# Optimization experiments

Measured on AMD Instinct MI355X. Metric: run time of the kernel, lower is better.

The kernel has to match this reference:

```python
import jax, jax.numpy as jnp
import numpy as np

ALPHA = 0.2  # leaky relu slope
NEG = -9e15

N, NFEAT, NHID, NHEADS = 4096, 1024, 64, 8
EMB = NHID * NHEADS  # 512


def setup_inputs() -> dict:
    key = jax.random.key(0)
    ks = jax.random.split(key, 16)
    x = jax.random.normal(ks[0], (N, NFEAT), dtype=jnp.float32)
    adj = (jax.random.uniform(ks[1], (N, N)) < 0.01).astype(jnp.float32)
    adj = jnp.maximum(adj, jnp.eye(N, dtype=jnp.float32))
    s = 0.05
    W = jax.random.normal(ks[2], (NHEADS, NFEAT, NHID), dtype=jnp.float32) * s
    a1 = jax.random.normal(ks[3], (NHEADS, NHID), dtype=jnp.float32) * s
    a2 = jax.random.normal(ks[4], (NHEADS, NHID), dtype=jnp.float32) * s
    # decoder: 512 -> 256 -> 256 -> 512 -> 1024 (PyTorch Linear convention: y = x @ W.T + b)
    W1 = jax.random.normal(ks[5], (EMB // 2, EMB), dtype=jnp.float32) * s
    b1 = jnp.zeros((EMB // 2,), dtype=jnp.float32)
    W2 = jax.random.normal(ks[6], (NFEAT // 4, EMB // 2), dtype=jnp.float32) * s
    b2 = jnp.zeros((NFEAT // 4,), dtype=jnp.float32)
    W3 = jax.random.normal(ks[7], (NFEAT // 2, NFEAT // 4), dtype=jnp.float32) * s
    b3 = jnp.zeros((NFEAT // 2,), dtype=jnp.float32)
    W4 = jax.random.normal(ks[8], (NFEAT, NFEAT // 2), dtype=jnp.float32) * s
    b4 = jnp.zeros((NFEAT,), dtype=jnp.float32)
    return {"x": x, "adj": adj, "W": W, "a1": a1, "a2": a2,
            "W1": W1, "b1": b1, "W2": W2, "b2": b2,
            "W3": W3, "b3": b3, "W4": W4, "b4": b4}


def reference(x, adj, W, a1, a2, W1, b1, W2, b2, W3, b3, W4, b4):
    # --- encoder: multi-head GAT (dropout=0) ---
    Wh = jnp.einsum('nf,hfd->hnd', x, W)              # [H, N, nhid]
    e_src = jnp.einsum('hnd,hd->hn', Wh, a1)          # [H, N]
    e_dst = jnp.einsum('hnd,hd->hn', Wh, a2)          # [H, N]
    e = jax.nn.leaky_relu(e_src[:, :, None] + e_dst[:, None, :], ALPHA)  # [H, N, N]
    e = jnp.where(adj[None] > 0, e, NEG)
    att = jax.nn.softmax(e, axis=-1)
    h = jnp.einsum('hnm,hmd->hnd', att, Wh)           # [H, N, nhid]
    h = jax.nn.elu(h)                                 # concat=True -> elu per layer
    enc = jnp.transpose(h, (1, 0, 2)).reshape(x.shape[0], -1)  # [N, H*nhid]
    # --- decoder: 4-layer MLP ---
    out = jax.nn.relu(enc @ W1.T + b1)
    out = jax.nn.relu(out @ W2.T + b2)
    out = jax.nn.relu(out @ W3.T + b3)
    out = out @ W4.T + b4
    return out
```

## Files before the change

kernel.cpp:

```cpp
#include <hip/hip_runtime.h>
#include <hip/hip_bf16.h>
#include <math.h>

#define NNODES 4096
#define NFEAT_ 1024
#define NHID_  64
#define NHEADS_ 8
#define EMB_   512
#define MAXD   256
constexpr float ALPHA_ = 0.2f;

typedef __attribute__((ext_vector_type(8))) short bf16x8;
typedef __attribute__((ext_vector_type(4))) float f32x4;
typedef unsigned int u32;
typedef unsigned short u16;

__device__ inline u16 f2b(float f) {
    __hip_bfloat16 b = __float2bfloat16(f);
    return *(u16*)&b;
}
__device__ inline float b2f(u16 u) {
    return __uint_as_float(((u32)u) << 16);
}

__device__ inline void cp16(const void* g, void* l) {
    __builtin_amdgcn_global_load_lds(
        (const __attribute__((address_space(1))) u32*)g,
        (__attribute__((address_space(3))) u32*)l, 16, 0, 0);
}

template<int BM, int BN, int OUTM, int ACT, bool SCORES>
__global__ __launch_bounds__(256) void gemm_bt(
    const u16* __restrict__ A, const u16* __restrict__ B,
    const float* __restrict__ bias, void* __restrict__ Cv,
    const float* __restrict__ a1, const float* __restrict__ a2,
    float* __restrict__ es, float* __restrict__ edT,
    int M, int N, int K)
{
    constexpr int BK  = 32;
    constexpr int WM  = BM / 2;
    constexpr int MI  = WM / 16;
    constexpr int WN  = BN / 2;
    constexpr int NJ  = WN / 16;
    constexpr int ACH = BM / 16;
    constexpr int BCH = BN / 16;
    static_assert(!SCORES || BN == 64, "SCORES assumes one head per block");

    __shared__ __align__(16) u16 As[2][BM * BK];
    __shared__ __align__(16) u16 Bs[2][BN * BK];
    __shared__ float s1Lds[SCORES ? 2 : 1][SCORES ? BM : 1];
    __shared__ float s2Lds[SCORES ? 2 : 1][SCORES ? BM : 1];

    const int tid  = threadIdx.x;
    const int wid  = tid >> 6, lane = tid & 63;
    const int wr   = wid >> 1, wc = wid & 1;
    const int m0   = blockIdx.y * BM, n0 = blockIdx.x * BN;
    const int frow = lane & 15, fk = (lane >> 4) * 8;
    const int lr   = lane >> 2, lc = (lane & 3) * 8;

    auto stage = [&](int buf, int k0) {
        const u16* gA = A + (long)m0 * K + k0;
        {
            int c = wid;
            cp16(gA + (long)(c * 16 + lr) * K + lc, &As[buf][c * 512]);
            if (ACH == 8) {
                c = wid + 4;
                cp16(gA + (long)(c * 16 + lr) * K + lc, &As[buf][c * 512]);
            }
        }
        const u16* gB = B + (long)n0 * K + k0;
        if (BCH >= 4) {
            int c = wid;
            cp16(gB + (long)(c * 16 + lr) * K + lc, &Bs[buf][c * 512]);
            if (BCH == 8) {
                c = wid + 4;
                cp16(gB + (long)(c * 16 + lr) * K + lc, &Bs[buf][c * 512]);
            }
        } else if (wid < BCH) {
            cp16(gB + (long)(wid * 16 + lr) * K + lc, &Bs[buf][wid * 512]);
        }
    };

    f32x4 acc[MI][NJ] = {};

    stage(0, 0);
    __syncthreads();
    int cur = 0;
    for (int k0 = 0; k0 < K; k0 += BK) {
        if (k0 + BK < K) stage(cur ^ 1, k0 + BK);

        bf16x8 af[MI], bfr[NJ];
        #pragma unroll
        for (int i = 0; i < MI; ++i)
            af[i] = *(const bf16x8*)&As[cur][(wr * WM + i * 16 + frow) * BK + fk];
        #pragma unroll
        for (int j = 0; j < NJ; ++j)
            bfr[j] = *(const bf16x8*)&Bs[cur][(wc * WN + j * 16 + frow) * BK + fk];
        #pragma unroll
        for (int i = 0; i < MI; ++i)
            #pragma unroll
            for (int j = 0; j < NJ; ++j)
                acc[i][j] = __builtin_amdgcn_mfma_f32_16x16x32_bf16(
                    af[i], bfr[j], acc[i][j], 0, 0, 0);

        __syncthreads();
        cur ^= 1;
    }

    const int crow0 = m0 + wr * WM + (lane >> 4) * 4;
    const int ccol0 = n0 + wc * WN + (lane & 15);
    #pragma unroll
    for (int i = 0; i < MI; ++i)
        #pragma unroll
        for (int j = 0; j < NJ; ++j)
            #pragma unroll
            for (int r = 0; r < 4; ++r) {
                const int row = crow0 + i * 16 + r;
                const int col = ccol0 + j * 16;
                float v = acc[i][j][r];
                if (bias) v += bias[col];
                if (ACT == 1) v = v > 0.f ? v : 0.f;
                if (OUTM == 1) ((u16*)Cv)[(long)row * N + col] = f2b(v);
                else           ((float*)Cv)[(long)row * N + col] = v;
            }

    if constexpr (SCORES) {
        const int h = n0 >> 6;
        const float a1v0 = a1[h * 64 + wc * WN + frow];
        const float a1v1 = a1[h * 64 + wc * WN + 16 + frow];
        const float a2v0 = a2[h * 64 + wc * WN + frow];
        const float a2v1 = a2[h * 64 + wc * WN + 16 + frow];
        #pragma unroll
        for (int i = 0; i < MI; ++i)
            #pragma unroll
            for (int r = 0; r < 4; ++r) {
                float s1 = acc[i][0][r] * a1v0 + acc[i][1][r] * a1v1;
                float s2 = acc[i][0][r] * a2v0 + acc[i][1][r] * a2v1;
                #pragma unroll
                for (int off = 8; off; off >>= 1) {
                    s1 += __shfl_xor(s1, off);
                    s2 += __shfl_xor(s2, off);
                }
                if (frow == 0) {
                    const int row = wr * WM + i * 16 + (lane >> 4) * 4 + r;
                    s1Lds[wc][row] = s1;
                    s2Lds[wc][row] = s2;
                }
            }
        __syncthreads();
        if (tid < BM) {
            es[h * NNODES + m0 + tid] = s1Lds[0][tid] + s1Lds[1][tid];
            edT[(m0 + tid) * NHEADS_ + h] = s2Lds[0][tid] + s2Lds[1][tid];
        }
    }
}

#define CASTB 512
__global__ __launch_bounds__(256) void prep_nbr(
    const float* __restrict__ x,   const float* __restrict__ adj,
    const float* __restrict__ W,
    const float* __restrict__ W1,  const float* __restrict__ W2,
    const float* __restrict__ W3,  const float* __restrict__ W4,
    u16* __restrict__ xb,  u16* __restrict__ WcT,
    u16* __restrict__ W1b, u16* __restrict__ W2b,
    u16* __restrict__ W3b, u16* __restrict__ W4b,
    int* __restrict__ cnt, int* __restrict__ nbr)
{
    const int b = blockIdx.x, tid = threadIdx.x;

    if (b < CASTB) {
        const int np = CASTB * 256;
        const int t = b * 256 + tid;
        for (int i = t; i < (NNODES * NFEAT_) / 4; i += np) {
            const float4 v = ((const float4*)x)[i];
            ushort4 o; o.x = f2b(v.x); o.y = f2b(v.y); o.z = f2b(v.z); o.w = f2b(v.w);
            ((ushort4*)xb)[i] = o;
        }
        for (int i = t; i < (256 * 512) / 4; i += np) {
            const float4 v = ((const float4*)W1)[i];
            ushort4 o; o.x = f2b(v.x); o.y = f2b(v.y); o.z = f2b(v.z); o.w = f2b(v.w);
            ((ushort4*)W1b)[i] = o;
        }
        for (int i = t; i < (256 * 256) / 4; i += np) {
            const float4 v = ((const float4*)W2)[i];
            ushort4 o; o.x = f2b(v.x); o.y = f2b(v.y); o.z = f2b(v.z); o.w = f2b(v.w);
            ((ushort4*)W2b)[i] = o;
        }
        for (int i = t; i < (512 * 256) / 4; i += np) {
            const float4 v = ((const float4*)W3)[i];
            ushort4 o; o.x = f2b(v.x); o.y = f2b(v.y); o.z = f2b(v.z); o.w = f2b(v.w);
            ((ushort4*)W3b)[i] = o;
        }
        for (int i = t; i < (1024 * 512) / 4; i += np) {
            const float4 v = ((const float4*)W4)[i];
            ushort4 o; o.x = f2b(v.x); o.y = f2b(v.y); o.z = f2b(v.z); o.w = f2b(v.w);
            ((ushort4*)W4b)[i] = o;
        }
    } else if (b < CASTB + 128) {
        __shared__ float tile[64][65];
        const int tb = b - CASTB;
        const int h = tb >> 4, k0 = (tb & 15) * 64;
        #pragma unroll
        for (int p = 0; p < 4; ++p) {
            const int kr = p * 16 + (tid >> 4), d = (tid & 15) * 4;
            const float4 v = *(const float4*)&W[((long)h * NFEAT_ + k0 + kr) * NHID_ + d];
            tile[kr][d] = v.x; tile[kr][d + 1] = v.y;
            tile[kr][d + 2] = v.z; tile[kr][d + 3] = v.w;
        }
        __syncthreads();
        #pragma unroll
        for (int p = 0; p < 4; ++p) {
            const int d = p * 16 + (tid >> 4), k = (tid & 15) * 4;
            ushort4 o;
            o.x = f2b(tile[k][d]);     o.y = f2b(tile[k + 1][d]);
            o.z = f2b(tile[k + 2][d]); o.w = f2b(tile[k + 3][d]);
            *(ushort4*)&WcT[((long)h * 64 + d) * NFEAT_ + k0 + k] = o;
        }
    } else {
        __shared__ int lcnt;
        const int n = b - CASTB - 128;
        if (tid == 0) lcnt = 0;
        __syncthreads();
        const float4* arow = (const float4*)(adj + (long)n * NNODES);
        for (int m4 = tid; m4 < NNODES / 4; m4 += 256) {
            const float4 v = arow[m4];
            if (v.x != 0.f) { const int p = atomicAdd(&lcnt, 1); if (p < MAXD) nbr[n * MAXD + p] = m4 * 4; }
            if (v.y != 0.f) { const int p = atomicAdd(&lcnt, 1); if (p < MAXD) nbr[n * MAXD + p] = m4 * 4 + 1; }
            if (v.z != 0.f) { const int p = atomicAdd(&lcnt, 1); if (p < MAXD) nbr[n * MAXD + p] = m4 * 4 + 2; }
            if (v.w != 0.f) { const int p = atomicAdd(&lcnt, 1); if (p < MAXD) nbr[n * MAXD + p] = m4 * 4 + 3; }
        }
        __syncthreads();
        if (tid == 0) cnt[n] = lcnt < MAXD ? lcnt : MAXD;
    }
}

__global__ __launch_bounds__(512) void attn_agg(
    const u16* __restrict__ Whb, const float* __restrict__ esrc,
    const float* __restrict__ edT, const int* __restrict__ cnt,
    const int* __restrict__ nbr, u16* __restrict__ enc)
{
    __shared__ __align__(16) int   mLds[MAXD];
    __shared__ __align__(16) float pLds[NHEADS_][MAXD];
    const int h = threadIdx.x >> 6, lane = threadIdx.x & 63;
    const int n = blockIdx.x;

    const int deg  = min(cnt[n], MAXD);
    const int degp = (deg + 15) & ~15;

    if (h == 0) {
        const int* lst = nbr + n * MAXD;
        for (int j = lane; j < deg; j += 64) mLds[j] = lst[j];
        for (int j = deg + lane; j < degp; j += 64) mLds[j] = 0;
    }
    __syncthreads();

    const float es = esrc[h * NNODES + n];

    float mymax = -3.4e38f;
    for (int j = lane; j < deg; j += 64) {
        float ev = es + edT[mLds[j] * NHEADS_ + h];
        ev = ev > 0.f ? ev : ALPHA_ * ev;
        pLds[h][j] = ev;
        mymax = fmaxf(mymax, ev);
    }
    for (int j = deg + lane; j < degp; j += 64) pLds[h][j] = 0.f;
    #pragma unroll
    for (int off = 32; off; off >>= 1) mymax = fmaxf(mymax, __shfl_xor(mymax, off));

    float mysum = 0.f;
    for (int j = lane; j < deg; j += 64) {
        const float p = __expf(pLds[h][j] - mymax);
        pLds[h][j] = p;
        mysum += p;
    }
    #pragma unroll
    for (int off = 32; off; off >>= 1) mysum += __shfl_xor(mysum, off);

    __syncthreads();

    float acc = 0.f;
    const u16* base = Whb + h * NHID_ + lane;
    for (int j0 = 0; j0 < degp; j0 += 16) {
        const int4   ma = *(const int4*)&mLds[j0];
        const int4   mb = *(const int4*)&mLds[j0 + 4];
        const int4   mc = *(const int4*)&mLds[j0 + 8];
        const int4   md = *(const int4*)&mLds[j0 + 12];
        const float4 pa = *(const float4*)&pLds[h][j0];
        const float4 pb = *(const float4*)&pLds[h][j0 + 4];
        const float4 pc = *(const float4*)&pLds[h][j0 + 8];
        const float4 pd = *(const float4*)&pLds[h][j0 + 12];
        const float v0  = b2f(base[(long)ma.x << 9]);
        const float v1  = b2f(base[(long)ma.y << 9]);
        const float v2  = b2f(base[(long)ma.z << 9]);
        const float v3  = b2f(base[(long)ma.w << 9]);
        const float v4  = b2f(base[(long)mb.x << 9]);
        const float v5  = b2f(base[(long)mb.y << 9]);
        const float v6  = b2f(base[(long)mb.z << 9]);
        const float v7  = b2f(base[(long)mb.w << 9]);
        const float v8  = b2f(base[(long)mc.x << 9]);
        const float v9  = b2f(base[(long)mc.y << 9]);
        const float v10 = b2f(base[(long)mc.z << 9]);
        const float v11 = b2f(base[(long)mc.w << 9]);
        const float v12 = b2f(base[(long)md.x << 9]);
        const float v13 = b2f(base[(long)md.y << 9]);
        const float v14 = b2f(base[(long)md.z << 9]);
        const float v15 = b2f(base[(long)md.w << 9]);
        acc = fmaf(pa.x, v0,  acc); acc = fmaf(pa.y, v1,  acc);
        acc = fmaf(pa.z, v2,  acc); acc = fmaf(pa.w, v3,  acc);
        acc = fmaf(pb.x, v4,  acc); acc = fmaf(pb.y, v5,  acc);
        acc = fmaf(pb.z, v6,  acc); acc = fmaf(pb.w, v7,  acc);
        acc = fmaf(pc.x, v8,  acc); acc = fmaf(pc.y, v9,  acc);
        acc = fmaf(pc.z, v10, acc); acc = fmaf(pc.w, v11, acc);
        acc = fmaf(pd.x, v12, acc); acc = fmaf(pd.y, v13, acc);
        acc = fmaf(pd.z, v14, acc); acc = fmaf(pd.w, v15, acc);
    }

    float hv = acc / mysum;
    hv = hv > 0.f ? hv : expm1f(hv);
    enc[(long)n * EMB_ + h * NHID_ + lane] = f2b(hv);
}

extern "C" void kernel_launch(void* const* d_in, const int* in_sizes, int n_in,
                              void* d_out, int out_size, void* d_ws, size_t ws_size,
                              hipStream_t stream)
{
    const float* x   = (const float*)d_in[0];
    const float* adj = (const float*)d_in[1];
    const float* W   = (const float*)d_in[2];
    const float* a1  = (const float*)d_in[3];
    const float* a2  = (const float*)d_in[4];
    const float* W1  = (const float*)d_in[5];
    const float* b1  = (const float*)d_in[6];
    const float* W2  = (const float*)d_in[7];
    const float* b2  = (const float*)d_in[8];
    const float* W3  = (const float*)d_in[9];
    const float* b3  = (const float*)d_in[10];
    const float* W4  = (const float*)d_in[11];
    const float* b4  = (const float*)d_in[12];
    float* out = (float*)d_out;

    float* es  = (float*)d_ws;
    float* edT = es + 32768;
    u16* Whb = (u16*)(edT + 32768);
    u16* enc = Whb + 2097152;
    u16* WcT = enc + 2097152;
    u16* W1b = WcT + 524288;
    u16* W2b = W1b + 131072;
    u16* W3b = W2b + 65536;
    u16* W4b = W3b + 131072;
    int* cnt = (int*)(W4b + 524288);
    int* nbr = cnt + 4096;
    u16* xb  = (u16*)(nbr + 1048576);
    u16* dd1 = xb;
    u16* dd2 = dd1 + 1048576;
    u16* dd3 = dd2 + 1048576;

    prep_nbr<<<dim3(CASTB + 128 + NNODES), 256, 0, stream>>>(
        x, adj, W, W1, W2, W3, W4, xb, WcT, W1b, W2b, W3b, W4b, cnt, nbr);

    gemm_bt<64, 64, 1, 0, true><<<dim3(8, 64), 256, 0, stream>>>(
        xb, WcT, nullptr, Whb, a1, a2, es, edT, NNODES, EMB_, NFEAT_);

    attn_agg<<<dim3(NNODES), 512, 0, stream>>>(Whb, es, edT, cnt, nbr, enc);

    gemm_bt<64, 32, 1, 1, false><<<dim3(8, 64), 256, 0, stream>>>(
        enc, W1b, b1, dd1, nullptr, nullptr, nullptr, nullptr, NNODES, 256, 512);
    gemm_bt<64, 32, 1, 1, false><<<dim3(8, 64), 256, 0, stream>>>(
        dd1, W2b, b2, dd2, nullptr, nullptr, nullptr, nullptr, NNODES, 256, 256);
    gemm_bt<64, 64, 1, 1, false><<<dim3(8, 64), 256, 0, stream>>>(
        dd2, W3b, b3, dd3, nullptr, nullptr, nullptr, nullptr, NNODES, 512, 256);
    gemm_bt<128, 128, 0, 0, false><<<dim3(8, 32), 256, 0, stream>>>(
        dd3, W4b, b4, out, nullptr, nullptr, nullptr, nullptr, NNODES, 1024, 512);
}
```

Baseline: 228.3 us.

## Move adjacency neighbor scan into head GEMM kernel and retile final decoder GEMM

```diff
diff --git a/kernel.cpp b/kernel.cpp
--- a/kernel.cpp
+++ b/kernel.cpp
@@ -29,12 +29,10 @@
         (__attribute__((address_space(3))) u32*)l, 16, 0, 0);
 }
 
-template<int BM, int BN, int OUTM, int ACT, bool SCORES>
+template<int BM, int BN, int OUTM, int ACT>
 __global__ __launch_bounds__(256) void gemm_bt(
     const u16* __restrict__ A, const u16* __restrict__ B,
     const float* __restrict__ bias, void* __restrict__ Cv,
-    const float* __restrict__ a1, const float* __restrict__ a2,
-    float* __restrict__ es, float* __restrict__ edT,
     int M, int N, int K)
 {
     constexpr int BK  = 32;
@@ -44,12 +42,9 @@
     constexpr int NJ  = WN / 16;
     constexpr int ACH = BM / 16;
     constexpr int BCH = BN / 16;
-    static_assert(!SCORES || BN == 64, "SCORES assumes one head per block");
 
     __shared__ __align__(16) u16 As[2][BM * BK];
     __shared__ __align__(16) u16 Bs[2][BN * BK];
-    __shared__ float s1Lds[SCORES ? 2 : 1][SCORES ? BM : 1];
-    __shared__ float s2Lds[SCORES ? 2 : 1][SCORES ? BM : 1];
 
     const int tid  = threadIdx.x;
     const int wid  = tid >> 6, lane = tid & 63;
@@ -123,102 +118,31 @@
                 if (OUTM == 1) ((u16*)Cv)[(long)row * N + col] = f2b(v);
                 else           ((float*)Cv)[(long)row * N + col] = v;
             }
-
-    if constexpr (SCORES) {
-        const int h = n0 >> 6;
-        const float a1v0 = a1[h * 64 + wc * WN + frow];
-        const float a1v1 = a1[h * 64 + wc * WN + 16 + frow];
-        const float a2v0 = a2[h * 64 + wc * WN + frow];
-        const float a2v1 = a2[h * 64 + wc * WN + 16 + frow];
-        #pragma unroll
-        for (int i = 0; i < MI; ++i)
-            #pragma unroll
-            for (int r = 0; r < 4; ++r) {
-                float s1 = acc[i][0][r] * a1v0 + acc[i][1][r] * a1v1;
-                float s2 = acc[i][0][r] * a2v0 + acc[i][1][r] * a2v1;
-                #pragma unroll
-                for (int off = 8; off; off >>= 1) {
-                    s1 += __shfl_xor(s1, off);
-                    s2 += __shfl_xor(s2, off);
-                }
-                if (frow == 0) {
-                    const int row = wr * WM + i * 16 + (lane >> 4) * 4 + r;
-                    s1Lds[wc][row] = s1;
-                    s2Lds[wc][row] = s2;
-                }
-            }
-        __syncthreads();
-        if (tid < BM) {
-            es[h * NNODES + m0 + tid] = s1Lds[0][tid] + s1Lds[1][tid];
-            edT[(m0 + tid) * NHEADS_ + h] = s2Lds[0][tid] + s2Lds[1][tid];
-        }
-    }
-}
-
-#define CASTB 512
-__global__ __launch_bounds__(256) void prep_nbr(
-    const float* __restrict__ x,   const float* __restrict__ adj,
-    const float* __restrict__ W,
-    const float* __restrict__ W1,  const float* __restrict__ W2,
-    const float* __restrict__ W3,  const float* __restrict__ W4,
-    u16* __restrict__ xb,  u16* __restrict__ WcT,
-    u16* __restrict__ W1b, u16* __restrict__ W2b,
-    u16* __restrict__ W3b, u16* __restrict__ W4b,
-    int* __restrict__ cnt, int* __restrict__ nbr)
+}
+
+__global__ __launch_bounds__(256) void head_gemm_nbr(
+    const u16* __restrict__ A, const u16* __restrict__ B,
+    u16* __restrict__ Whb,
+    const float* __restrict__ a1, const float* __restrict__ a2,
+    float* __restrict__ es, float* __restrict__ edT,
+    const float* __restrict__ adj, int* __restrict__ cnt,
+    int* __restrict__ nbr)
 {
-    const int b = blockIdx.x, tid = threadIdx.x;
-
-    if (b < CASTB) {
-        const int np = CASTB * 256;
-        const int t = b * 256 + tid;
-        for (int i = t; i < (NNODES * NFEAT_) / 4; i += np) {
-            const float4 v = ((const float4*)x)[i];
-            ushort4 o; o.x = f2b(v.x); o.y = f2b(v.y); o.z = f2b(v.z); o.w = f2b(v.w);
-            ((ushort4*)xb)[i] = o;
-        }
-        for (int i = t; i < (256 * 512) / 4; i += np) {
-            const float4 v = ((const float4*)W1)[i];
-            ushort4 o; o.x = f2b(v.x); o.y = f2b(v.y); o.z = f2b(v.z); o.w = f2b(v.w);
-            ((ushort4*)W1b)[i] = o;
-        }
-        for (int i = t; i < (256 * 256) / 4; i += np) {
-            const float4 v = ((const float4*)W2)[i];
-            ushort4 o; o.x = f2b(v.x); o.y = f2b(v.y); o.z = f2b(v.z); o.w = f2b(v.w);
-            ((ushort4*)W2b)[i] = o;
-        }
-        for (int i = t; i < (512 * 256) / 4; i += np) {
-            const float4 v = ((const float4*)W3)[i];
-            ushort4 o; o.x = f2b(v.x); o.y = f2b(v.y); o.z = f2b(v.z); o.w = f2b(v.w);
-            ((ushort4*)W3b)[i] = o;
-        }
-        for (int i = t; i < (1024 * 512) / 4; i += np) {
-            const float4 v = ((const float4*)W4)[i];
-            ushort4 o; o.x = f2b(v.x); o.y = f2b(v.y); o.z = f2b(v.z); o.w = f2b(v.w);
-            ((ushort4*)W4b)[i] = o;
-        }
-    } else if (b < CASTB + 128) {
-        __shared__ float tile[64][65];
-        const int tb = b - CASTB;
-        const int h = tb >> 4, k0 = (tb & 15) * 64;
-        #pragma unroll
-        for (int p = 0; p < 4; ++p) {
-            const int kr = p * 16 + (tid >> 4), d = (tid & 15) * 4;
-            const float4 v = *(const float4*)&W[((long)h * NFEAT_ + k0 + kr) * NHID_ + d];
-            tile[kr][d] = v.x; tile[kr][d + 1] = v.y;
-            tile[kr][d + 2] = v.z; tile[kr][d + 3] = v.w;
-        }
-        __syncthreads();
-        #pragma unroll
-        for (int p = 0; p < 4; ++p) {
-            const int d = p * 16 + (tid >> 4), k = (tid & 15) * 4;
-            ushort4 o;
-            o.x = f2b(tile[k][d]);     o.y = f2b(tile[k + 1][d]);
-            o.z = f2b(tile[k + 2][d]); o.w = f2b(tile[k + 3][d]);
-            *(ushort4*)&WcT[((long)h * 64 + d) * NFEAT_ + k0 + k] = o;
-        }
-    } else {
-        __shared__ int lcnt;
-        const int n = b - CASTB - 128;
+    constexpr int BM = 64, BN = 64, BK = 32;
+    constexpr int WM = 32, MI = 2, WN = 32, NJ = 2;
+    constexpr int M = NNODES, N = EMB_, K = NFEAT_;
+
+    __shared__ __align__(16) u16 As[2][BM * BK];
+    __shared__ __align__(16) u16 Bs[2][BN * BK];
+    __shared__ float s1Lds[2][BM];
+    __shared__ float s2Lds[2][BM];
+    __shared__ int lcnt;
+
+    const int bid = blockIdx.x;
+    const int tid = threadIdx.x;
+
+    if (bid >= 512) {
+        const int n = bid - 512;
         if (tid == 0) lcnt = 0;
         __syncthreads();
         const float4* arow = (const float4*)(adj + (long)n * NNODES);
@@ -231,6 +155,147 @@
         }
         __syncthreads();
         if (tid == 0) cnt[n] = lcnt < MAXD ? lcnt : MAXD;
+        return;
+    }
+
+    const int wid  = tid >> 6, lane = tid & 63;
+    const int wr   = wid >> 1, wc = wid & 1;
+    const int m0   = (bid >> 3) * BM, n0 = (bid & 7) * BN;
+    const int frow = lane & 15, fk = (lane >> 4) * 8;
+    const int lr   = lane >> 2, lc = (lane & 3) * 8;
+
+    auto stage = [&](int buf, int k0) {
+        const u16* gA = A + (long)m0 * K + k0;
+        cp16(gA + (long)(wid * 16 + lr) * K + lc, &As[buf][wid * 512]);
+        const u16* gB = B + (long)n0 * K + k0;
+        cp16(gB + (long)(wid * 16 + lr) * K + lc, &Bs[buf][wid * 512]);
+    };
+
+    f32x4 acc[MI][NJ] = {};
+
+    stage(0, 0);
+    __syncthreads();
+    int cur = 0;
+    for (int k0 = 0; k0 < K; k0 += BK) {
+        if (k0 + BK < K) stage(cur ^ 1, k0 + BK);
+
+        bf16x8 af[MI], bfr[NJ];
+        #pragma unroll
+        for (int i = 0; i < MI; ++i)
+            af[i] = *(const bf16x8*)&As[cur][(wr * WM + i * 16 + frow) * BK + fk];
+        #pragma unroll
+        for (int j = 0; j < NJ; ++j)
+            bfr[j] = *(const bf16x8*)&Bs[cur][(wc * WN + j * 16 + frow) * BK + fk];
+        #pragma unroll
+        for (int i = 0; i < MI; ++i)
+            #pragma unroll
+            for (int j = 0; j < NJ; ++j)
+                acc[i][j] = __builtin_amdgcn_mfma_f32_16x16x32_bf16(
+                    af[i], bfr[j], acc[i][j], 0, 0, 0);
+
+        __syncthreads();
+        cur ^= 1;
+    }
+
+    const int crow0 = m0 + wr * WM + (lane >> 4) * 4;
+    const int ccol0 = n0 + wc * WN + (lane & 15);
+    #pragma unroll
+    for (int i = 0; i < MI; ++i)
+        #pragma unroll
+        for (int j = 0; j < NJ; ++j)
+            #pragma unroll
+            for (int r = 0; r < 4; ++r)
+                Whb[(long)(crow0 + i * 16 + r) * N + ccol0 + j * 16] =
+                    f2b(acc[i][j][r]);
+
+    const int h = n0 >> 6;
+    const float a1v0 = a1[h * 64 + wc * WN + frow];
+    const float a1v1 = a1[h * 64 + wc * WN + 16 + frow];
+    const float a2v0 = a2[h * 64 + wc * WN + frow];
+    const float a2v1 = a2[h * 64 + wc * WN + 16 + frow];
+    #pragma unroll
+    for (int i = 0; i < MI; ++i)
+        #pragma unroll
+        for (int r = 0; r < 4; ++r) {
+            float s1 = acc[i][0][r] * a1v0 + acc[i][1][r] * a1v1;
+            float s2 = acc[i][0][r] * a2v0 + acc[i][1][r] * a2v1;
+            #pragma unroll
+            for (int off = 8; off; off >>= 1) {
+                s1 += __shfl_xor(s1, off);
+                s2 += __shfl_xor(s2, off);
+            }
+            if (frow == 0) {
+                const int row = wr * WM + i * 16 + (lane >> 4) * 4 + r;
+                s1Lds[wc][row] = s1;
+                s2Lds[wc][row] = s2;
+            }
+        }
+    __syncthreads();
+    if (tid < BM) {
+        es[h * NNODES + m0 + tid] = s1Lds[0][tid] + s1Lds[1][tid];
+        edT[(m0 + tid) * NHEADS_ + h] = s2Lds[0][tid] + s2Lds[1][tid];
+    }
+}
+
+#define CASTB 512
+__global__ __launch_bounds__(256) void prep(
+    const float* __restrict__ x,   const float* __restrict__ W,
+    const float* __restrict__ W1,  const float* __restrict__ W2,
+    const float* __restrict__ W3,  const float* __restrict__ W4,
+    u16* __restrict__ xb,  u16* __restrict__ WcT,
+    u16* __restrict__ W1b, u16* __restrict__ W2b,
+    u16* __restrict__ W3b, u16* __restrict__ W4b)
+{
+    const int b = blockIdx.x, tid = threadIdx.x;
+
+    if (b < CASTB) {
+        const int np = CASTB * 256;
+        const int t = b * 256 + tid;
+        for (int i = t; i < (NNODES * NFEAT_) / 4; i += np) {
+            const float4 v = ((const float4*)x)[i];
+            ushort4 o; o.x = f2b(v.x); o.y = f2b(v.y); o.z = f2b(v.z); o.w = f2b(v.w);
+            ((ushort4*)xb)[i] = o;
+        }
+        for (int i = t; i < (256 * 512) / 4; i += np) {
+            const float4 v = ((const float4*)W1)[i];
+            ushort4 o; o.x = f2b(v.x); o.y = f2b(v.y); o.z = f2b(v.z); o.w = f2b(v.w);
+            ((ushort4*)W1b)[i] = o;
+        }
+        for (int i = t; i < (256 * 256) / 4; i += np) {
+            const float4 v = ((const float4*)W2)[i];
+            ushort4 o; o.x = f2b(v.x); o.y = f2b(v.y); o.z = f2b(v.z); o.w = f2b(v.w);
+            ((ushort4*)W2b)[i] = o;
+        }
+        for (int i = t; i < (512 * 256) / 4; i += np) {
+            const float4 v = ((const float4*)W3)[i];
+            ushort4 o; o.x = f2b(v.x); o.y = f2b(v.y); o.z = f2b(v.z); o.w = f2b(v.w);
+            ((ushort4*)W3b)[i] = o;
+        }
+        for (int i = t; i < (1024 * 512) / 4; i += np) {
+            const float4 v = ((const float4*)W4)[i];
+            ushort4 o; o.x = f2b(v.x); o.y = f2b(v.y); o.z = f2b(v.z); o.w = f2b(v.w);
+            ((ushort4*)W4b)[i] = o;
+        }
+    } else {
+        __shared__ float tile[64][65];
+        const int tb = b - CASTB;
+        const int h = tb >> 4, k0 = (tb & 15) * 64;
+        #pragma unroll
+        for (int p = 0; p < 4; ++p) {
+            const int kr = p * 16 + (tid >> 4), d = (tid & 15) * 4;
+            const float4 v = *(const float4*)&W[((long)h * NFEAT_ + k0 + kr) * NHID_ + d];
+            tile[kr][d] = v.x; tile[kr][d + 1] = v.y;
+            tile[kr][d + 2] = v.z; tile[kr][d + 3] = v.w;
+        }
+        __syncthreads();
+        #pragma unroll
+        for (int p = 0; p < 4; ++p) {
+            const int d = p * 16 + (tid >> 4), k = (tid & 15) * 4;
+            ushort4 o;
+            o.x = f2b(tile[k][d]);     o.y = f2b(tile[k + 1][d]);
+            o.z = f2b(tile[k + 2][d]); o.w = f2b(tile[k + 3][d]);
+            *(ushort4*)&WcT[((long)h * 64 + d) * NFEAT_ + k0 + k] = o;
+        }
     }
 }
 
@@ -355,20 +420,20 @@
     u16* dd2 = dd1 + 1048576;
     u16* dd3 = dd2 + 1048576;
 
-    prep_nbr<<<dim3(CASTB + 128 + NNODES), 256, 0, stream>>>(
-        x, adj, W, W1, W2, W3, W4, xb, WcT, W1b, W2b, W3b, W4b, cnt, nbr);
-
-    gemm_bt<64, 64, 1, 0, true><<<dim3(8, 64), 256, 0, stream>>>(
-        xb, WcT, nullptr, Whb, a1, a2, es, edT, NNODES, EMB_, NFEAT_);
+    prep<<<dim3(CASTB + 128), 256, 0, stream>>>(
+        x, W, W1, W2, W3, W4, xb, WcT, W1b, W2b, W3b, W4b);
+
+    head_gemm_nbr<<<dim3(512 + NNODES), 256, 0, stream>>>(
+        xb, WcT, Whb, a1, a2, es, edT, adj, cnt, nbr);
 
     attn_agg<<<dim3(NNODES), 512, 0, stream>>>(Whb, es, edT, cnt, nbr, enc);
 
-    gemm_bt<64, 32, 1, 1, false><<<dim3(8, 64), 256, 0, stream>>>(
-        enc, W1b, b1, dd1, nullptr, nullptr, nullptr, nullptr, NNODES, 256, 512);
-    gemm_bt<64, 32, 1, 1, false><<<dim3(8, 64), 256, 0, stream>>>(
-        dd1, W2b, b2, dd2, nullptr, nullptr, nullptr, nullptr, NNODES, 256, 256);
-    gemm_bt<64, 64, 1, 1, false><<<dim3(8, 64), 256, 0, stream>>>(
-        dd2, W3b, b3, dd3, nullptr, nullptr, nullptr, nullptr, NNODES, 512, 256);
-    gemm_bt<128, 128, 0, 0, false><<<dim3(8, 32), 256, 0, stream>>>(
-        dd3, W4b, b4, out, nullptr, nullptr, nullptr, nullptr, NNODES, 1024, 512);
-}
+    gemm_bt<64, 32, 1, 1><<<dim3(8, 64), 256, 0, stream>>>(
+        enc, W1b, b1, dd1, NNODES, 256, 512);
+    gemm_bt<64, 32, 1, 1><<<dim3(8, 64), 256, 0, stream>>>(
+        dd1, W2b, b2, dd2, NNODES, 256, 256);
+    gemm_bt<64, 64, 1, 1><<<dim3(8, 64), 256, 0, stream>>>(
+        dd2, W3b, b3, dd3, NNODES, 512, 256);
+    gemm_bt<64, 128, 0, 0><<<dim3(8, 64), 256, 0, stream>>>(
+        dd3, W4b, b4, out, NNODES, 1024, 512);
+}
```

After: 222.1 us. -2.7%, faster.
